# Kernel optimization log

Hardware: AMD Instinct MI355X
Metric: run time of the kernel (lower is better)

## Reference

```python
import jax, jax.numpy as jnp
import numpy as np

N = 100000   # nodes
E = 600000   # edges
F_IN = 128
F_OUT = 128


def setup_inputs() -> dict:
    key = jax.random.key(0)
    k1, k2, k3, k4 = jax.random.split(key, 4)
    x = jax.random.normal(k1, (N, F_IN), dtype=jnp.float32)
    edge_index = jax.random.randint(k2, (2, E), 0, N, dtype=jnp.int32)
    edge_wt = jnp.ones((E,), dtype=jnp.float32)  # learnable param, init ones
    # GCNConv weight (glorot-ish scale) and bias
    weight = jax.random.normal(k3, (F_IN, F_OUT), dtype=jnp.float32) / np.sqrt(F_IN).astype(np.float32)
    bias = jnp.zeros((F_OUT,), dtype=jnp.float32)
    u = jax.random.normal(k4, (F_IN,), dtype=jnp.float32)  # spectral-norm power-iter buffer
    return {"x": x, "edge_index": edge_index, "edge_wt": edge_wt,
            "weight": weight, "bias": bias, "u": u}


def _l2norm(v):
    return v / (jnp.linalg.norm(v) + 1e-12)


def reference(x, edge_index, edge_wt, weight, bias, u):
    # --- spectral norm on GCNConv weight (one power iteration, torch semantics:
    # u, v are stop-gradiented buffers; sigma = u^T W v keeps grad wrt W) ---
    W_sg = jax.lax.stop_gradient(weight)
    v = _l2norm(W_sg.T @ jax.lax.stop_gradient(u))
    u1 = _l2norm(W_sg @ v)
    sigma = u1 @ (weight @ v)
    W_sn = weight / sigma

    # --- per-edge sigmoid-weighted GCNConv with self loops + symmetric norm ---
    w = jax.nn.sigmoid(edge_wt)                      # [E]
    row, col = edge_index[0], edge_index[1]
    loop = jnp.arange(N, dtype=edge_index.dtype)
    row_a = jnp.concatenate([row, loop])             # [E+N]
    col_a = jnp.concatenate([col, loop])
    w_a = jnp.concatenate([w, jnp.ones((N,), w.dtype)])  # self-loop weight 1

    deg = jax.ops.segment_sum(w_a, col_a, num_segments=N)   # [N]
    dinv = jnp.where(deg > 0, deg ** -0.5, 0.0)
    norm = dinv[row_a] * w_a * dinv[col_a]           # [E+N]

    xw = x @ W_sn                                    # [N, F_OUT]
    msgs = norm[:, None] * xw[row_a]                 # [E+N, F_OUT] gather
    out = jax.ops.segment_sum(msgs, col_a, num_segments=N) + bias  # scatter
    return out
```

## Files before the change

### kernel.cpp

```cpp
#include <hip/hip_runtime.h>
#include <math.h>

#define F 128

typedef __bf16 bf16_t;
typedef unsigned long long u64;
typedef __attribute__((ext_vector_type(8))) bf16_t bf16x8;
typedef __attribute__((ext_vector_type(4))) bf16_t bf16x4;
typedef __attribute__((ext_vector_type(4))) float floatx4;

#define DEG_SCALE 32768.0f
#define DEG_INV   (1.0f / 32768.0f)

__global__ __launch_bounds__(256) void init_spec_k(const float* __restrict__ W,
                                                   const float* __restrict__ u,
                                                   bf16_t* __restrict__ Wt,
                                                   unsigned* __restrict__ dc, int n) {
    if (blockIdx.x == 0) {
        __shared__ float Wl[F][F + 1];
        __shared__ float ul[F];
        __shared__ float sv[F];
        __shared__ float red[4];
        __shared__ float snorm, s_is;
        int t = threadIdx.x;
        if (t < F) ul[t] = u[t];
        for (int i = t; i < F * 32; i += 256) {
            int r = i >> 5, c4 = (i & 31) * 4;
            float4 v = *(const float4*)(W + r * F + c4);
            Wl[r][c4] = v.x; Wl[r][c4 + 1] = v.y; Wl[r][c4 + 2] = v.z; Wl[r][c4 + 3] = v.w;
        }
        __syncthreads();
        float s = 0.f;
        if (t < F)
            for (int i = 0; i < F; ++i) s += Wl[i][t] * ul[i];
        float ss = (t < F) ? s * s : 0.f;
        for (int o = 32; o > 0; o >>= 1) ss += __shfl_down(ss, o);
        if ((t & 63) == 0) red[t >> 6] = ss;
        __syncthreads();
        if (t == 0) snorm = sqrtf(red[0] + red[1] + red[2] + red[3]);
        __syncthreads();
        if (t < F) sv[t] = s / (snorm + 1e-12f);
        __syncthreads();
        float s2 = 0.f;
        if (t < F)
            for (int j = 0; j < F; ++j) s2 += Wl[t][j] * sv[j];
        float ss2 = (t < F) ? s2 * s2 : 0.f;
        for (int o = 32; o > 0; o >>= 1) ss2 += __shfl_down(ss2, o);
        if ((t & 63) == 0) red[t >> 6] = ss2;
        __syncthreads();
        if (t == 0) {
            float a = red[0] + red[1] + red[2] + red[3];
            float nt = sqrtf(a);
            float sigma = a / (nt + 1e-12f);
            s_is = 1.0f / sigma;
        }
        __syncthreads();
        float is = s_is;
        for (int i = t; i < F * 16; i += 256) {
            int nrow = i >> 4, c = (i & 15) * 8;
            bf16x8 v;
#pragma unroll
            for (int j = 0; j < 8; ++j) v[j] = (bf16_t)(Wl[c + j][nrow] * is);
            *(bf16x8*)(Wt + nrow * F + c) = v;
        }
    } else {
        int i = (blockIdx.x - 1) * 256 + threadIdx.x;
        if (i < n) dc[i] = 0u;
    }
}

#define GBMW 16
#define LDK 136
__global__ __launch_bounds__(64) void count_gemm_k(const int* __restrict__ col,
                                                   const float* __restrict__ wt,
                                                   unsigned* __restrict__ dc,
                                                   int* __restrict__ rank, int e_cnt,
                                                   const float* __restrict__ x,
                                                   const bf16_t* __restrict__ Wt,
                                                   bf16_t* __restrict__ xwh, int nrows,
                                                   int gGemm) {
    __shared__ bf16_t Os[GBMW * LDK];
    int b = blockIdx.x;
    int lane = threadIdx.x;
    if (b >= gGemm) {
        int e4 = ((b - gGemm) * 64 + lane) * 4;
        if (e4 + 3 < e_cnt) {
            int4 c = *(const int4*)(col + e4);
            float4 w = *(const float4*)(wt + e4);
            unsigned p0 = (1u << 24) | (unsigned)rintf(DEG_SCALE / (1.0f + expf(-w.x)));
            unsigned p1 = (1u << 24) | (unsigned)rintf(DEG_SCALE / (1.0f + expf(-w.y)));
            unsigned p2 = (1u << 24) | (unsigned)rintf(DEG_SCALE / (1.0f + expf(-w.z)));
            unsigned p3 = (1u << 24) | (unsigned)rintf(DEG_SCALE / (1.0f + expf(-w.w)));
            unsigned o0 = atomicAdd(dc + c.x, p0);
            unsigned o1 = atomicAdd(dc + c.y, p1);
            unsigned o2 = atomicAdd(dc + c.z, p2);
            unsigned o3 = atomicAdd(dc + c.w, p3);
            *(int4*)(rank + e4) = make_int4((int)(o0 >> 24), (int)(o1 >> 24),
                                            (int)(o2 >> 24), (int)(o3 >> 24));
        } else {
            for (int e = e4; e < e_cnt && e < e4 + 4; ++e) {
                int c = col[e];
                unsigned pkt = (1u << 24) | (unsigned)rintf(DEG_SCALE / (1.0f + expf(-wt[e])));
                unsigned old = atomicAdd(dc + c, pkt);
                rank[e] = (int)(old >> 24);
            }
        }
        return;
    }
    int l16 = lane & 15, q = lane >> 4;
    int wRow = b * GBMW;

    int arow = wRow + l16;
    bool rok = (arow < nrows);
    const float* xrow = x + (size_t)(rok ? arow : 0) * F;

    float4 r0[4], r1[4];
#pragma unroll
    for (int kt = 0; kt < 4; ++kt) {
        r0[kt] = make_float4(0.f, 0.f, 0.f, 0.f);
        r1[kt] = r0[kt];
        if (rok) {
            r0[kt] = *(const float4*)(xrow + kt * 32 + q * 8);
            r1[kt] = *(const float4*)(xrow + kt * 32 + q * 8 + 4);
        }
    }
    bf16x8 a[4];
#pragma unroll
    for (int kt = 0; kt < 4; ++kt) {
        bf16x8 v;
        v[0] = (bf16_t)r0[kt].x; v[1] = (bf16_t)r0[kt].y;
        v[2] = (bf16_t)r0[kt].z; v[3] = (bf16_t)r0[kt].w;
        v[4] = (bf16_t)r1[kt].x; v[5] = (bf16_t)r1[kt].y;
        v[6] = (bf16_t)r1[kt].z; v[7] = (bf16_t)r1[kt].w;
        a[kt] = v;
    }

    floatx4 acc[8];
#pragma unroll
    for (int nt = 0; nt < 8; ++nt) acc[nt] = (floatx4){0.f, 0.f, 0.f, 0.f};

#pragma unroll
    for (int kt = 0; kt < 4; ++kt) {
#pragma unroll
        for (int nt = 0; nt < 8; ++nt) {
            bf16x8 bb = *(const bf16x8*)(Wt + (size_t)(nt * 16 + l16) * F + kt * 32 + q * 8);
            acc[nt] = __builtin_amdgcn_mfma_f32_16x16x32_bf16(a[kt], bb, acc[nt], 0, 0, 0);
        }
    }

#pragma unroll
    for (int nt = 0; nt < 8; ++nt) {
#pragma unroll
        for (int r = 0; r < 4; ++r)
            Os[(q * 4 + r) * LDK + nt * 16 + l16] = (bf16_t)acc[nt][r];
    }
#pragma unroll
    for (int j = 0; j < 4; ++j) {
        int idx = j * 64 + lane;
        int r = idx >> 4, c8 = (idx & 15) * 8;
        int grow = wRow + r;
        if (grow < nrows)
            *(bf16x8*)(xwh + (size_t)grow * F + c8) = *(bf16x8*)(Os + r * LDK + c8);
    }
}

#define STILE 1024
__global__ __launch_bounds__(256) void scan1_k(const unsigned* __restrict__ dc,
                                               int* __restrict__ bsum,
                                               float* __restrict__ dinv, int n) {
    __shared__ int red[256];
    int t = threadIdx.x;
    int base = blockIdx.x * STILE + t * 4;
    int s = 0;
    for (int i = 0; i < 4; ++i) {
        if (base + i < n) {
            unsigned v = dc[base + i];
            s += (int)(v >> 24);
            float d = 1.0f + (float)(v & 0xFFFFFFu) * DEG_INV;
            dinv[base + i] = 1.0f / sqrtf(d);
        }
    }
    red[t] = s;
    __syncthreads();
    for (int o = 128; o > 0; o >>= 1) { if (t < o) red[t] += red[t + o]; __syncthreads(); }
    if (t == 0) bsum[blockIdx.x] = red[0];
}

__global__ __launch_bounds__(256) void scan3_k(const unsigned* __restrict__ dc,
                                               const int* __restrict__ bsum,
                                               int* __restrict__ offsets, int g, int n) {
    __shared__ int sc[256];
    int t = threadIdx.x;
    int bid = blockIdx.x;
    int bbase = 0;
    for (int i = 0; i < bid; ++i) bbase += bsum[i];
    int base = bid * STILE + t * 4;
    int v[4] = {0, 0, 0, 0};
    for (int i = 0; i < 4; ++i)
        if (base + i < n) v[i] = (int)(dc[base + i] >> 24);
    int ts = v[0] + v[1] + v[2] + v[3];
    sc[t] = ts;
    __syncthreads();
    for (int o = 1; o < 256; o <<= 1) {
        int val = sc[t];
        int add = (t >= o) ? sc[t - o] : 0;
        __syncthreads();
        sc[t] = val + add;
        __syncthreads();
    }
    int run = bbase + sc[t] - ts;
    for (int i = 0; i < 4; ++i) {
        if (base + i < n) offsets[base + i] = run;
        run += v[i];
    }
    if (bid == g - 1 && t == 255) offsets[n] = bbase + sc[255];
}

__global__ __launch_bounds__(256) void fill_k(const int* __restrict__ row,
                                              const int* __restrict__ col,
                                              const float* __restrict__ wt,
                                              const float* __restrict__ dinv,
                                              const int* __restrict__ offsets,
                                              const int* __restrict__ rank,
                                              int2* __restrict__ edat, int e_cnt) {
    int e = blockIdx.x * 256 + threadIdx.x;
    if (e < e_cnt) {
        int r = row[e], c = col[e];
        float w = 1.0f / (1.0f + expf(-wt[e]));
        float nv = dinv[r] * w * dinv[c];
        int p = offsets[c] + rank[e];
        edat[p] = make_int2(r, __float_as_int(nv));
    }
}

template <int MODE>
__global__ __launch_bounds__(256) void gather_t(const int* __restrict__ offsets,
                                                const int2* __restrict__ edat,
                                                const float* __restrict__ dinv,
                                                const float* __restrict__ x,
                                                const bf16_t* __restrict__ xh,
                                                const float* __restrict__ bias,
                                                float* __restrict__ out, int n) {
    int node = blockIdx.x * 4 + (threadIdx.x >> 6);
    if (node >= n) return;
    int lane = threadIdx.x & 63;
    const float2* x2 = (const float2*)x;
    float dv = dinv[node];
    float2 acc;
    if (MODE) {
        unsigned vs = ((const unsigned*)(xh + (size_t)node * F))[lane];
        acc.x = dv * dv * __uint_as_float(vs << 16);
        acc.y = dv * dv * __uint_as_float(vs & 0xFFFF0000u);
    } else {
        float2 xv = x2[(size_t)node * 64 + lane];
        acc.x = dv * dv * xv.x;
        acc.y = dv * dv * xv.y;
    }
    int s = offsets[node], e = offsets[node + 1];
    for (int b = s; b < e; b += 64) {
        int cnt = min(64, e - b);
        int2 ed = make_int2(0, 0);
        if (lane < cnt) ed = edat[b + lane];
        int j = 0;
        for (; j + 4 <= cnt; j += 4) {
            int r0 = __shfl(ed.x, j + 0), r1 = __shfl(ed.x, j + 1);
            int r2 = __shfl(ed.x, j + 2), r3 = __shfl(ed.x, j + 3);
            float n0 = __int_as_float(__shfl(ed.y, j + 0));
            float n1 = __int_as_float(__shfl(ed.y, j + 1));
            float n2 = __int_as_float(__shfl(ed.y, j + 2));
            float n3 = __int_as_float(__shfl(ed.y, j + 3));
            if (MODE) {
                unsigned v0 = ((const unsigned*)(xh + (size_t)r0 * F))[lane];
                unsigned v1 = ((const unsigned*)(xh + (size_t)r1 * F))[lane];
                unsigned v2 = ((const unsigned*)(xh + (size_t)r2 * F))[lane];
                unsigned v3 = ((const unsigned*)(xh + (size_t)r3 * F))[lane];
                acc.x = fmaf(n0, __uint_as_float(v0 << 16), acc.x);
                acc.y = fmaf(n0, __uint_as_float(v0 & 0xFFFF0000u), acc.y);
                acc.x = fmaf(n1, __uint_as_float(v1 << 16), acc.x);
                acc.y = fmaf(n1, __uint_as_float(v1 & 0xFFFF0000u), acc.y);
                acc.x = fmaf(n2, __uint_as_float(v2 << 16), acc.x);
                acc.y = fmaf(n2, __uint_as_float(v2 & 0xFFFF0000u), acc.y);
                acc.x = fmaf(n3, __uint_as_float(v3 << 16), acc.x);
                acc.y = fmaf(n3, __uint_as_float(v3 & 0xFFFF0000u), acc.y);
            } else {
                float2 a0 = x2[(size_t)r0 * 64 + lane];
                float2 a1 = x2[(size_t)r1 * 64 + lane];
                float2 a2 = x2[(size_t)r2 * 64 + lane];
                float2 a3 = x2[(size_t)r3 * 64 + lane];
                acc.x = fmaf(n0, a0.x, acc.x); acc.y = fmaf(n0, a0.y, acc.y);
                acc.x = fmaf(n1, a1.x, acc.x); acc.y = fmaf(n1, a1.y, acc.y);
                acc.x = fmaf(n2, a2.x, acc.x); acc.y = fmaf(n2, a2.y, acc.y);
                acc.x = fmaf(n3, a3.x, acc.x); acc.y = fmaf(n3, a3.y, acc.y);
            }
        }
        for (; j < cnt; ++j) {
            int r = __shfl(ed.x, j);
            float nv = __int_as_float(__shfl(ed.y, j));
            if (MODE) {
                unsigned v = ((const unsigned*)(xh + (size_t)r * F))[lane];
                acc.x = fmaf(nv, __uint_as_float(v << 16), acc.x);
                acc.y = fmaf(nv, __uint_as_float(v & 0xFFFF0000u), acc.y);
            } else {
                float2 xr = x2[(size_t)r * 64 + lane];
                acc.x = fmaf(nv, xr.x, acc.x);
                acc.y = fmaf(nv, xr.y, acc.y);
            }
        }
    }
    if (MODE) {
        float2 bv = ((const float2*)bias)[lane];
        acc.x += bv.x;
        acc.y += bv.y;
    }
    ((float2*)out)[(size_t)node * 64 + lane] = acc;
}

#define GBM 64
__global__ __launch_bounds__(256) void gemm_mfma_k(float* __restrict__ io,
                                                   const bf16_t* __restrict__ Wt,
                                                   const float* __restrict__ bias,
                                                   int nrows) {
    __shared__ bf16_t As[GBM * LDK];
    int tid = threadIdx.x;
    int rowBase = blockIdx.x * GBM;

    for (int i = tid; i < GBM * 32; i += 256) {
        int r = i >> 5, c4 = (i & 31) * 4;
        float4 xv = make_float4(0.f, 0.f, 0.f, 0.f);
        if (rowBase + r < nrows) xv = *(const float4*)(io + (size_t)(rowBase + r) * F + c4);
        bf16x4 v;
        v.x = (bf16_t)xv.x; v.y = (bf16_t)xv.y; v.z = (bf16_t)xv.z; v.w = (bf16_t)xv.w;
        *(bf16x4*)(As + r * LDK + c4) = v;
    }
    __syncthreads();

    int wave = tid >> 6, lane = tid & 63;
    int l16 = lane & 15, q = lane >> 4;
    int mrow = wave * 16;

    floatx4 acc[8];
#pragma unroll
    for (int nt = 0; nt < 8; ++nt) acc[nt] = (floatx4){0.f, 0.f, 0.f, 0.f};

#pragma unroll
    for (int kt = 0; kt < 4; ++kt) {
        bf16x8 a = *(bf16x8*)(As + (mrow + l16) * LDK + kt * 32 + q * 8);
#pragma unroll
        for (int nt = 0; nt < 8; ++nt) {
            bf16x8 b = *(const bf16x8*)(Wt + (size_t)(nt * 16 + l16) * F + kt * 32 + q * 8);
            acc[nt] = __builtin_amdgcn_mfma_f32_16x16x32_bf16(a, b, acc[nt], 0, 0, 0);
        }
    }

#pragma unroll
    for (int nt = 0; nt < 8; ++nt) {
        int col = nt * 16 + l16;
        float bv = bias[col];
#pragma unroll
        for (int r = 0; r < 4; ++r) {
            int grow = rowBase + mrow + q * 4 + r;
            if (grow < nrows) io[(size_t)grow * F + col] = acc[nt][r] + bv;
        }
    }
}

extern "C" void kernel_launch(void* const* d_in, const int* in_sizes, int n_in,
                              void* d_out, int out_size, void* d_ws, size_t ws_size,
                              hipStream_t stream) {
    const float* x    = (const float*)d_in[0];
    const int*   ei   = (const int*)d_in[1];
    const float* ewt  = (const float*)d_in[2];
    const float* W    = (const float*)d_in[3];
    const float* bias = (const float*)d_in[4];
    const float* u    = (const float*)d_in[5];
    float* out = (float*)d_out;

    int n_nodes = in_sizes[0] / F;
    int e_cnt   = in_sizes[2];
    const int* row = ei;
    const int* col = ei + e_cnt;

    char* wsb = (char*)d_ws;
    float*    dinv    = (float*)wsb;
    size_t off = ((size_t)n_nodes * 4 + 15) & ~(size_t)15;
    unsigned* dc      = (unsigned*)(wsb + off);
    off += (size_t)n_nodes * 4;
    off = (off + 15) & ~(size_t)15;
    int*      offsets = (int*)(wsb + off);
    off += (size_t)(n_nodes + 1) * 4;
    off = (off + 15) & ~(size_t)15;
    int*      bsum    = (int*)(wsb + off);
    off += 2048 * 4;
    off = (off + 15) & ~(size_t)15;
    int*      rank    = (int*)(wsb + off);
    off += (size_t)e_cnt * 4;
    off = (off + 15) & ~(size_t)15;
    int2*     edat    = (int2*)(wsb + off);
    off += (size_t)e_cnt * 8;
    off = (off + 15) & ~(size_t)15;
    bf16_t*   Wt      = (bf16_t*)(wsb + off);
    off += (size_t)F * F * 2;
    bf16_t*   xwh     = (bf16_t*)(wsb + off);
    size_t need_bf16 = off + (size_t)n_nodes * F * 2;
    int use_bf16 = (ws_size >= need_bf16);

    int g_scan  = (n_nodes + STILE - 1) / STILE;
    int gCount  = (e_cnt + 255) / 256;
    int gInit   = (n_nodes + 255) / 256;
    int gGemm   = (n_nodes + GBMW - 1) / GBMW;
    int gGemmF  = (n_nodes + GBM - 1) / GBM;

    init_spec_k<<<gInit + 1, 256, 0, stream>>>(W, u, Wt, dc, n_nodes);
    if (use_bf16) {
        count_gemm_k<<<gGemm + gCount, 64, 0, stream>>>(col, ewt, dc, rank, e_cnt, x, Wt,
                                                        xwh, n_nodes, gGemm);
    } else {
        count_gemm_k<<<gCount, 64, 0, stream>>>(col, ewt, dc, rank, e_cnt, x, Wt,
                                                xwh, n_nodes, 0);
    }
    scan1_k<<<g_scan, 256, 0, stream>>>(dc, bsum, dinv, n_nodes);
    scan3_k<<<g_scan, 256, 0, stream>>>(dc, bsum, offsets, g_scan, n_nodes);
    fill_k<<<(e_cnt + 255) / 256, 256, 0, stream>>>(row, col, ewt, dinv, offsets, rank,
                                                    edat, e_cnt);
    if (use_bf16) {
        gather_t<1><<<(n_nodes + 3) / 4, 256, 0, stream>>>(offsets, edat, dinv, x, xwh, bias,
                                                           out, n_nodes);
    } else {
        gather_t<0><<<(n_nodes + 3) / 4, 256, 0, stream>>>(offsets, edat, dinv, x, xwh, bias,
                                                           out, n_nodes);
        gemm_mfma_k<<<gGemmF, 256, 0, stream>>>(out, Wt, bias, n_nodes);
    }
}
```

Measured before the change: 219.8 us.

## Spread x@W GEMM tiles across count, scan and fill kernels

The dense xW GEMM used to run entirely inside the degree-count kernel. Its 64-row tiles are now split into four chunks, each appended to one of the count, scan1, scan3 and fill launches. The aim is to fill the otherwise underused, latency-bound scan and fill kernels with independent compute. The count path also moves from 64-thread to 256-thread blocks, and the GEMM blocks now use 4 waves each. This adds shared-memory use to the scan kernels, which can reduce their occupancy, and ties GEMM progress to the launch order.

Measured after the change: 233.3 us. 1.06x slower.

```diff
diff --git a/kernel.cpp b/kernel.cpp
--- a/kernel.cpp
+++ b/kernel.cpp
@@ -11,6 +11,69 @@
 
 #define DEG_SCALE 32768.0f
 #define DEG_INV   (1.0f / 32768.0f)
+
+#define GBM 64
+#define GBMW 16
+#define LDK 136
+#define STILE 1024
+
+__device__ __forceinline__ void gemm_tile_wave(const float* __restrict__ x,
+                                               const bf16_t* __restrict__ Wt,
+                                               bf16_t* __restrict__ xwh, int nrows,
+                                               bf16_t* Os, int wRow, int lane) {
+    int l16 = lane & 15, q = lane >> 4;
+    int arow = wRow + l16;
+    bool rok = (arow < nrows);
+    const float* xrow = x + (size_t)(rok ? arow : 0) * F;
+
+    float4 r0[4], r1[4];
+#pragma unroll
+    for (int kt = 0; kt < 4; ++kt) {
+        r0[kt] = make_float4(0.f, 0.f, 0.f, 0.f);
+        r1[kt] = r0[kt];
+        if (rok) {
+            r0[kt] = *(const float4*)(xrow + kt * 32 + q * 8);
+            r1[kt] = *(const float4*)(xrow + kt * 32 + q * 8 + 4);
+        }
+    }
+    bf16x8 a[4];
+#pragma unroll
+    for (int kt = 0; kt < 4; ++kt) {
+        bf16x8 v;
+        v[0] = (bf16_t)r0[kt].x; v[1] = (bf16_t)r0[kt].y;
+        v[2] = (bf16_t)r0[kt].z; v[3] = (bf16_t)r0[kt].w;
+        v[4] = (bf16_t)r1[kt].x; v[5] = (bf16_t)r1[kt].y;
+        v[6] = (bf16_t)r1[kt].z; v[7] = (bf16_t)r1[kt].w;
+        a[kt] = v;
+    }
+
+    floatx4 acc[8];
+#pragma unroll
+    for (int nt = 0; nt < 8; ++nt) acc[nt] = (floatx4){0.f, 0.f, 0.f, 0.f};
+#pragma unroll
+    for (int kt = 0; kt < 4; ++kt) {
+#pragma unroll
+        for (int nt = 0; nt < 8; ++nt) {
+            bf16x8 bb = *(const bf16x8*)(Wt + (size_t)(nt * 16 + l16) * F + kt * 32 + q * 8);
+            acc[nt] = __builtin_amdgcn_mfma_f32_16x16x32_bf16(a[kt], bb, acc[nt], 0, 0, 0);
+        }
+    }
+
+#pragma unroll
+    for (int nt = 0; nt < 8; ++nt) {
+#pragma unroll
+        for (int r = 0; r < 4; ++r)
+            Os[(q * 4 + r) * LDK + nt * 16 + l16] = (bf16_t)acc[nt][r];
+    }
+#pragma unroll
+    for (int j = 0; j < 4; ++j) {
+        int idx = j * 64 + lane;
+        int r = idx >> 4, c8 = (idx & 15) * 8;
+        int grow = wRow + r;
+        if (grow < nrows)
+            *(bf16x8*)(xwh + (size_t)grow * F + c8) = *(bf16x8*)(Os + r * LDK + c8);
+    }
+}
 
 __global__ __launch_bounds__(256) void init_spec_k(const float* __restrict__ W,
                                                    const float* __restrict__ u,
@@ -69,108 +132,63 @@
     }
 }
 
-#define GBMW 16
-#define LDK 136
-__global__ __launch_bounds__(64) void count_gemm_k(const int* __restrict__ col,
-                                                   const float* __restrict__ wt,
-                                                   unsigned* __restrict__ dc,
-                                                   int* __restrict__ rank, int e_cnt,
-                                                   const float* __restrict__ x,
-                                                   const bf16_t* __restrict__ Wt,
-                                                   bf16_t* __restrict__ xwh, int nrows,
-                                                   int gGemm) {
-    __shared__ bf16_t Os[GBMW * LDK];
-    int b = blockIdx.x;
-    int lane = threadIdx.x;
-    if (b >= gGemm) {
-        int e4 = ((b - gGemm) * 64 + lane) * 4;
-        if (e4 + 3 < e_cnt) {
-            int4 c = *(const int4*)(col + e4);
-            float4 w = *(const float4*)(wt + e4);
-            unsigned p0 = (1u << 24) | (unsigned)rintf(DEG_SCALE / (1.0f + expf(-w.x)));
-            unsigned p1 = (1u << 24) | (unsigned)rintf(DEG_SCALE / (1.0f + expf(-w.y)));
-            unsigned p2 = (1u << 24) | (unsigned)rintf(DEG_SCALE / (1.0f + expf(-w.z)));
-            unsigned p3 = (1u << 24) | (unsigned)rintf(DEG_SCALE / (1.0f + expf(-w.w)));
-            unsigned o0 = atomicAdd(dc + c.x, p0);
-            unsigned o1 = atomicAdd(dc + c.y, p1);
-            unsigned o2 = atomicAdd(dc + c.z, p2);
-            unsigned o3 = atomicAdd(dc + c.w, p3);
-            *(int4*)(rank + e4) = make_int4((int)(o0 >> 24), (int)(o1 >> 24),
-                                            (int)(o2 >> 24), (int)(o3 >> 24));
-        } else {
-            for (int e = e4; e < e_cnt && e < e4 + 4; ++e) {
-                int c = col[e];
-                unsigned pkt = (1u << 24) | (unsigned)rintf(DEG_SCALE / (1.0f + expf(-wt[e])));
-                unsigned old = atomicAdd(dc + c, pkt);
-                rank[e] = (int)(old >> 24);
-            }
-        }
+__global__ __launch_bounds__(256) void count_gemm_k(const int* __restrict__ col,
+                                                    const float* __restrict__ wt,
+                                                    unsigned* __restrict__ dc,
+                                                    int* __restrict__ rank, int e_cnt,
+                                                    const float* __restrict__ x,
+                                                    const bf16_t* __restrict__ Wt,
+                                                    bf16_t* __restrict__ xwh, int nrows,
+                                                    int tileLo, int nGemm) {
+    __shared__ bf16_t Os[4][GBMW * LDK];
+    int b = blockIdx.x, tid = threadIdx.x;
+    if (b < nGemm) {
+        int wave = tid >> 6, lane = tid & 63;
+        gemm_tile_wave(x, Wt, xwh, nrows, Os[wave],
+                       (tileLo + b) * GBM + wave * GBMW, lane);
         return;
     }
-    int l16 = lane & 15, q = lane >> 4;
-    int wRow = b * GBMW;
-
-    int arow = wRow + l16;
-    bool rok = (arow < nrows);
-    const float* xrow = x + (size_t)(rok ? arow : 0) * F;
-
-    float4 r0[4], r1[4];
-#pragma unroll
-    for (int kt = 0; kt < 4; ++kt) {
-        r0[kt] = make_float4(0.f, 0.f, 0.f, 0.f);
-        r1[kt] = r0[kt];
-        if (rok) {
-            r0[kt] = *(const float4*)(xrow + kt * 32 + q * 8);
-            r1[kt] = *(const float4*)(xrow + kt * 32 + q * 8 + 4);
-        }
-    }
-    bf16x8 a[4];
-#pragma unroll
-    for (int kt = 0; kt < 4; ++kt) {
-        bf16x8 v;
-        v[0] = (bf16_t)r0[kt].x; v[1] = (bf16_t)r0[kt].y;
-        v[2] = (bf16_t)r0[kt].z; v[3] = (bf16_t)r0[kt].w;
-        v[4] = (bf16_t)r1[kt].x; v[5] = (bf16_t)r1[kt].y;
-        v[6] = (bf16_t)r1[kt].z; v[7] = (bf16_t)r1[kt].w;
-        a[kt] = v;
-    }
-
-    floatx4 acc[8];
-#pragma unroll
-    for (int nt = 0; nt < 8; ++nt) acc[nt] = (floatx4){0.f, 0.f, 0.f, 0.f};
-
-#pragma unroll
-    for (int kt = 0; kt < 4; ++kt) {
-#pragma unroll
-        for (int nt = 0; nt < 8; ++nt) {
-            bf16x8 bb = *(const bf16x8*)(Wt + (size_t)(nt * 16 + l16) * F + kt * 32 + q * 8);
-            acc[nt] = __builtin_amdgcn_mfma_f32_16x16x32_bf16(a[kt], bb, acc[nt], 0, 0, 0);
-        }
-    }
-
-#pragma unroll
-    for (int nt = 0; nt < 8; ++nt) {
-#pragma unroll
-        for (int r = 0; r < 4; ++r)
-            Os[(q * 4 + r) * LDK + nt * 16 + l16] = (bf16_t)acc[nt][r];
-    }
-#pragma unroll
-    for (int j = 0; j < 4; ++j) {
-        int idx = j * 64 + lane;
-        int r = idx >> 4, c8 = (idx & 15) * 8;
-        int grow = wRow + r;
-        if (grow < nrows)
-            *(bf16x8*)(xwh + (size_t)grow * F + c8) = *(bf16x8*)(Os + r * LDK + c8);
-    }
-}
-
-#define STILE 1024
-__global__ __launch_bounds__(256) void scan1_k(const unsigned* __restrict__ dc,
-                                               int* __restrict__ bsum,
-                                               float* __restrict__ dinv, int n) {
+    int e4 = ((b - nGemm) * 256 + tid) * 4;
+    if (e4 + 3 < e_cnt) {
+        int4 c = *(const int4*)(col + e4);
+        float4 w = *(const float4*)(wt + e4);
+        unsigned p0 = (1u << 24) | (unsigned)rintf(DEG_SCALE / (1.0f + expf(-w.x)));
+        unsigned p1 = (1u << 24) | (unsigned)rintf(DEG_SCALE / (1.0f + expf(-w.y)));
+        unsigned p2 = (1u << 24) | (unsigned)rintf(DEG_SCALE / (1.0f + expf(-w.z)));
+        unsigned p3 = (1u << 24) | (unsigned)rintf(DEG_SCALE / (1.0f + expf(-w.w)));
+        unsigned o0 = atomicAdd(dc + c.x, p0);
+        unsigned o1 = atomicAdd(dc + c.y, p1);
+        unsigned o2 = atomicAdd(dc + c.z, p2);
+        unsigned o3 = atomicAdd(dc + c.w, p3);
+        *(int4*)(rank + e4) = make_int4((int)(o0 >> 24), (int)(o1 >> 24),
+                                        (int)(o2 >> 24), (int)(o3 >> 24));
+    } else {
+        for (int e = e4; e < e_cnt && e < e4 + 4; ++e) {
+            int c = col[e];
+            unsigned pkt = (1u << 24) | (unsigned)rintf(DEG_SCALE / (1.0f + expf(-wt[e])));
+            unsigned old = atomicAdd(dc + c, pkt);
+            rank[e] = (int)(old >> 24);
+        }
+    }
+}
+
+__global__ __launch_bounds__(256) void scan1_gemm_k(const unsigned* __restrict__ dc,
+                                                    int* __restrict__ bsum,
+                                                    float* __restrict__ dinv, int n,
+                                                    const float* __restrict__ x,
+                                                    const bf16_t* __restrict__ Wt,
+                                                    bf16_t* __restrict__ xwh, int nrows,
+                                                    int tileLo, int g_scan) {
+    int b = blockIdx.x, t = threadIdx.x;
+    if (b >= g_scan) {
+        __shared__ bf16_t Os[4][GBMW * LDK];
+        int wave = t >> 6, lane = t & 63;
+        gemm_tile_wave(x, Wt, xwh, nrows, Os[wave],
+                       (tileLo + (b - g_scan)) * GBM + wave * GBMW, lane);
+        return;
+    }
     __shared__ int red[256];
-    int t = threadIdx.x;
-    int base = blockIdx.x * STILE + t * 4;
+    int base = b * STILE + t * 4;
     int s = 0;
     for (int i = 0; i < 4; ++i) {
         if (base + i < n) {
@@ -183,18 +201,29 @@
     red[t] = s;
     __syncthreads();
     for (int o = 128; o > 0; o >>= 1) { if (t < o) red[t] += red[t + o]; __syncthreads(); }
-    if (t == 0) bsum[blockIdx.x] = red[0];
-}
-
-__global__ __launch_bounds__(256) void scan3_k(const unsigned* __restrict__ dc,
-                                               const int* __restrict__ bsum,
-                                               int* __restrict__ offsets, int g, int n) {
+    if (t == 0) bsum[b] = red[0];
+}
+
+__global__ __launch_bounds__(256) void scan3_gemm_k(const unsigned* __restrict__ dc,
+                                                    const int* __restrict__ bsum,
+                                                    int* __restrict__ offsets,
+                                                    int g_scan, int n,
+                                                    const float* __restrict__ x,
+                                                    const bf16_t* __restrict__ Wt,
+                                                    bf16_t* __restrict__ xwh, int nrows,
+                                                    int tileLo) {
+    int b = blockIdx.x, t = threadIdx.x;
+    if (b >= g_scan) {
+        __shared__ bf16_t Os[4][GBMW * LDK];
+        int wave = t >> 6, lane = t & 63;
+        gemm_tile_wave(x, Wt, xwh, nrows, Os[wave],
+                       (tileLo + (b - g_scan)) * GBM + wave * GBMW, lane);
+        return;
+    }
     __shared__ int sc[256];
-    int t = threadIdx.x;
-    int bid = blockIdx.x;
     int bbase = 0;
-    for (int i = 0; i < bid; ++i) bbase += bsum[i];
-    int base = bid * STILE + t * 4;
+    for (int i = 0; i < b; ++i) bbase += bsum[i];
+    int base = b * STILE + t * 4;
     int v[4] = {0, 0, 0, 0};
     for (int i = 0; i < 4; ++i)
         if (base + i < n) v[i] = (int)(dc[base + i] >> 24);
@@ -213,17 +242,29 @@
         if (base + i < n) offsets[base + i] = run;
         run += v[i];
     }
-    if (bid == g - 1 && t == 255) offsets[n] = bbase + sc[255];
-}
-
-__global__ __launch_bounds__(256) void fill_k(const int* __restrict__ row,
-                                              const int* __restrict__ col,
-                                              const float* __restrict__ wt,
-                                              const float* __restrict__ dinv,
-                                              const int* __restrict__ offsets,
-                                              const int* __restrict__ rank,
-                                              int2* __restrict__ edat, int e_cnt) {
-    int e = blockIdx.x * 256 + threadIdx.x;
+    if (b == g_scan - 1 && t == 255) offsets[n] = bbase + sc[255];
+}
+
+__global__ __launch_bounds__(256) void fill_gemm_k(const int* __restrict__ row,
+                                                   const int* __restrict__ col,
+                                                   const float* __restrict__ wt,
+                                                   const float* __restrict__ dinv,
+                                                   const int* __restrict__ offsets,
+                                                   const int* __restrict__ rank,
+                                                   int2* __restrict__ edat, int e_cnt,
+                                                   const float* __restrict__ x,
+                                                   const bf16_t* __restrict__ Wt,
+                                                   bf16_t* __restrict__ xwh, int nrows,
+                                                   int tileLo, int nFill) {
+    int b = blockIdx.x, t = threadIdx.x;
+    if (b >= nFill) {
+        __shared__ bf16_t Os[4][GBMW * LDK];
+        int wave = t >> 6, lane = t & 63;
+        gemm_tile_wave(x, Wt, xwh, nrows, Os[wave],
+                       (tileLo + (b - nFill)) * GBM + wave * GBMW, lane);
+        return;
+    }
+    int e = b * 256 + t;
     if (e < e_cnt) {
         int r = row[e], c = col[e];
         float w = 1.0f / (1.0f + expf(-wt[e]));
@@ -315,7 +356,6 @@
     ((float2*)out)[(size_t)node * 64 + lane] = acc;
 }
 
-#define GBM 64
 __global__ __launch_bounds__(256) void gemm_mfma_k(float* __restrict__ io,
                                                    const bf16_t* __restrict__ Wt,
                                                    const float* __restrict__ bias,
@@ -405,29 +445,35 @@
     int use_bf16 = (ws_size >= need_bf16);
 
     int g_scan  = (n_nodes + STILE - 1) / STILE;
-    int gCount  = (e_cnt + 255) / 256;
+    int gCount  = (e_cnt + 1023) / 1024;
     int gInit   = (n_nodes + 255) / 256;
-    int gGemm   = (n_nodes + GBMW - 1) / GBMW;
-    int gGemmF  = (n_nodes + GBM - 1) / GBM;
+    int gFill   = (e_cnt + 255) / 256;
+    int tiles64 = (n_nodes + GBM - 1) / GBM;
+
+    int cA = (tiles64 + 3) / 4;
+    int cB = cA, cC = cA;
+    int cD = tiles64 - cA - cB - cC;
+    if (cD < 0) { cD = 0; }
+    if (!use_bf16) { cA = cB = cC = cD = 0; }
+    int loA = 0, loB = cA, loC = cA + cB, loD = cA + cB + cC;
+    int nrows_g = use_bf16 ? n_nodes : 0;
 
     init_spec_k<<<gInit + 1, 256, 0, stream>>>(W, u, Wt, dc, n_nodes);
-    if (use_bf16) {
-        count_gemm_k<<<gGemm + gCount, 64, 0, stream>>>(col, ewt, dc, rank, e_cnt, x, Wt,
-                                                        xwh, n_nodes, gGemm);
-    } else {
-        count_gemm_k<<<gCount, 64, 0, stream>>>(col, ewt, dc, rank, e_cnt, x, Wt,
-                                                xwh, n_nodes, 0);
-    }
-    scan1_k<<<g_scan, 256, 0, stream>>>(dc, bsum, dinv, n_nodes);
-    scan3_k<<<g_scan, 256, 0, stream>>>(dc, bsum, offsets, g_scan, n_nodes);
-    fill_k<<<(e_cnt + 255) / 256, 256, 0, stream>>>(row, col, ewt, dinv, offsets, rank,
-                                                    edat, e_cnt);
+    count_gemm_k<<<cA + gCount, 256, 0, stream>>>(col, ewt, dc, rank, e_cnt,
+                                                  x, Wt, xwh, nrows_g, loA, cA);
+    scan1_gemm_k<<<g_scan + cB, 256, 0, stream>>>(dc, bsum, dinv, n_nodes,
+                                                  x, Wt, xwh, nrows_g, loB, g_scan);
+    scan3_gemm_k<<<g_scan + cC, 256, 0, stream>>>(dc, bsum, offsets, g_scan, n_nodes,
+                                                  x, Wt, xwh, nrows_g, loC);
+    fill_gemm_k<<<gFill + cD, 256, 0, stream>>>(row, col, ewt, dinv, offsets, rank,
+                                                edat, e_cnt, x, Wt, xwh, nrows_g,
+                                                loD, gFill);
     if (use_bf16) {
         gather_t<1><<<(n_nodes + 3) / 4, 256, 0, stream>>>(offsets, edat, dinv, x, xwh, bias,
                                                            out, n_nodes);
     } else {
         gather_t<0><<<(n_nodes + 3) / 4, 256, 0, stream>>>(offsets, edat, dinv, x, xwh, bias,
                                                            out, n_nodes);
-        gemm_mfma_k<<<gGemmF, 256, 0, stream>>>(out, Wt, bias, n_nodes);
-    }
-}
+        gemm_mfma_k<<<tiles64, 256, 0, stream>>>(out, Wt, bias, n_nodes);
+    }
+}
```
